# Kernel optimization log

Measured on AMD Instinct MI355X. Metric: run time of the kernel, lower is better.

Reference implementation:

```python
import jax, jax.numpy as jnp
import numpy as np

N, E, NODE_DIM, EDGE_DIM, H, L, G = 50000, 800000, 128, 16, 64, 3, 64


def setup_inputs() -> dict:
    key = jax.random.key(0)
    ks = jax.random.split(key, 20)
    s = 0.05
    inp = {
        "x": jax.random.normal(ks[0], (N, NODE_DIM), jnp.float32),
        "edge_index": jax.random.randint(ks[1], (2, E), 0, N, jnp.int32),
        "edge_attr": jax.random.normal(ks[2], (E, EDGE_DIM), jnp.float32),
        "batch": jnp.sort(jax.random.randint(ks[3], (N,), 0, G, jnp.int32)),
        # node embedding
        "emb_w": jax.random.normal(ks[4], (NODE_DIM, H), jnp.float32) * s,
        "emb_b": jnp.zeros((H,), jnp.float32),
        # per-layer message MLP (stacked over layers)
        "msg_w1": jax.random.normal(ks[5], (L, 2 * H + EDGE_DIM, H), jnp.float32) * s,
        "msg_b1": jnp.zeros((L, H), jnp.float32),
        "msg_w2": jax.random.normal(ks[6], (L, H, H), jnp.float32) * s,
        "msg_b2": jnp.zeros((L, H), jnp.float32),
        # per-layer GRUCell params (torch layout: [3H, H] = [r|z|n])
        "gru_wih": jax.random.normal(ks[7], (L, 3 * H, H), jnp.float32) * s,
        "gru_whh": jax.random.normal(ks[8], (L, 3 * H, H), jnp.float32) * s,
        "gru_bih": jnp.zeros((L, 3 * H), jnp.float32),
        "gru_bhh": jnp.zeros((L, 3 * H), jnp.float32),
        # readout
        "ro_w1": jax.random.normal(ks[9], (H, H), jnp.float32) * s,
        "ro_b1": jnp.zeros((H,), jnp.float32),
        "ro_w2": jax.random.normal(ks[10], (H, 1), jnp.float32) * s,
        "ro_b2": jnp.zeros((1,), jnp.float32),
    }
    return inp


def _layer(x, row, col, edge_attr, w1, b1, w2, b2, wih, whh, bih, bhh):
    # gather-concat-MLP: m is [E, 2H+EDGE_DIM]
    m = jnp.concatenate([x[row], x[col], edge_attr], axis=-1)
    m = jax.nn.relu(m @ w1 + b1) @ w2 + b2  # [E, H]
    agg = jax.ops.segment_sum(m, row, num_segments=N)  # scatter-add -> [N, H]
    # GRUCell(agg, x): gates in torch order r, z, n
    gi = agg @ wih.T + bih  # [N, 3H]
    gh = x @ whh.T + bhh    # [N, 3H]
    r = jax.nn.sigmoid(gi[:, :H] + gh[:, :H])
    z = jax.nn.sigmoid(gi[:, H:2 * H] + gh[:, H:2 * H])
    n = jnp.tanh(gi[:, 2 * H:] + r * gh[:, 2 * H:])
    return (1.0 - z) * n + z * x


def reference(x, edge_index, edge_attr, batch, emb_w, emb_b,
              msg_w1, msg_b1, msg_w2, msg_b2,
              gru_wih, gru_whh, gru_bih, gru_bhh,
              ro_w1, ro_b1, ro_w2, ro_b2):
    row, col = edge_index[0], edge_index[1]
    h = x @ emb_w + emb_b  # node embedding [N, H]
    for l in range(L):
        h = _layer(h, row, col, edge_attr,
                   msg_w1[l], msg_b1[l], msg_w2[l], msg_b2[l],
                   gru_wih[l], gru_whh[l], gru_bih[l], gru_bhh[l])
    # global mean pool over graphs
    sums = jax.ops.segment_sum(h, batch, num_segments=G)
    counts = jax.ops.segment_sum(jnp.ones((N,), h.dtype), batch, num_segments=G)
    g = sums / jnp.maximum(counts, 1.0)[:, None]  # [G, H]
    # readout (dropout is identity in eval mode)
    out = jax.nn.sigmoid(jax.nn.relu(g @ ro_w1 + ro_b1) @ ro_w2 + ro_b2)
    return out  # [G, 1]
```

## Files before the change

### kernel.cpp

```cpp
#include <hip/hip_runtime.h>
#include <cstdint>

#define NN 50000
#define NE 800000
#define HD 64
#define ED 16
#define XD 128
#define NL 3
#define NG 64
#define H3 192
#define POOL_SLICES 16

typedef unsigned int uint32;
typedef unsigned short ushort16;

#if __has_builtin(__builtin_amdgcn_fdot2)
#define USE_DOT2 1
typedef _Float16 v2h __attribute__((ext_vector_type(2)));
#else
#define USE_DOT2 0
#endif

static __device__ __forceinline__ float sigm(float x){ return 1.0f/(1.0f+expf(-x)); }

static __device__ __forceinline__ uint32 f2bf_bits(float f){
  uint32 u = __float_as_uint(f);
  return (u + 0x7fffu + ((u>>16)&1u)) >> 16;
}
static __device__ __forceinline__ uint32 pack2bf(float a, float b){
  return f2bf_bits(a) | (f2bf_bits(b) << 16);
}
static __device__ __forceinline__ float bf_lo(uint32 u){ return __uint_as_float(u << 16); }
static __device__ __forceinline__ float bf_hi(uint32 u){ return __uint_as_float(u & 0xffff0000u); }

#if USE_DOT2
static __device__ __forceinline__ uint32 pack2h(float a, float b){
  v2h p = {(_Float16)a, (_Float16)b};
  return __builtin_bit_cast(uint32, p);
}
static __device__ __forceinline__ float dot2h(uint32 a, uint32 b, float c){
  return __builtin_amdgcn_fdot2(__builtin_bit_cast(v2h, a), __builtin_bit_cast(v2h, b), c, false);
}
#endif

static __device__ __forceinline__ void pre_from_lds(const float* hW, int ldh,
    const float* __restrict__ w1, const float* __restrict__ b1,
    int nb, int lane, float* __restrict__ m1, ushort16* __restrict__ m2b){
  float a1[8] = {0,0,0,0,0,0,0,0};
  float a2[8] = {0,0,0,0,0,0,0,0};
  #pragma unroll 4
  for (int kq=0;kq<HD/4;kq++){
    float wa[4], wb[4];
    #pragma unroll
    for (int q=0;q<4;q++){
      wa[q] = w1[(kq*4+q)*HD + lane];
      wb[q] = w1[(HD+kq*4+q)*HD + lane];
    }
    #pragma unroll
    for (int n=0;n<8;n++){
      float hk[4];
      *(float4*)hk = *(const float4*)&hW[n*ldh + kq*4];
      #pragma unroll
      for (int q=0;q<4;q++){
        a1[n] = fmaf(hk[q], wa[q], a1[n]);
        a2[n] = fmaf(hk[q], wb[q], a2[n]);
      }
    }
  }
  float bb = b1[lane];
  #pragma unroll
  for (int n=0;n<8;n++){
    m1[(size_t)(nb+n)*HD + lane] = a1[n] + bb;
    m2b[(size_t)(nb+n)*HD + lane] = (ushort16)f2bf_bits(a2[n]);
  }
}

__global__ __launch_bounds__(256) void k_embed_pre(const float* __restrict__ x,
    const float* __restrict__ w, const float* __restrict__ b,
    const float* __restrict__ w1_0, const float* __restrict__ b1_0,
    float* __restrict__ h, float* __restrict__ m1, ushort16* __restrict__ m2b){
  __shared__ float xL[4][8][XD];
  int w4 = threadIdx.x >> 6, lane = threadIdx.x & 63;
  int nb = blockIdx.x*32 + w4*8;
  if (nb >= NN) return;
  #pragma unroll
  for (int n=0;n<8;n++){
    xL[w4][n][lane]      = x[(size_t)(nb+n)*XD + lane];
    xL[w4][n][64+lane]   = x[(size_t)(nb+n)*XD + 64 + lane];
  }
  float a[8] = {0,0,0,0,0,0,0,0};
  #pragma unroll 4
  for (int kq=0;kq<XD/4;kq++){
    float wv[4];
    #pragma unroll
    for (int q=0;q<4;q++) wv[q] = w[(kq*4+q)*HD + lane];
    #pragma unroll
    for (int n=0;n<8;n++){
      float xk[4];
      *(float4*)xk = *(const float4*)&xL[w4][n][kq*4];
      #pragma unroll
      for (int q=0;q<4;q++) a[n] = fmaf(xk[q], wv[q], a[n]);
    }
  }
  float bb = b[lane];
  #pragma unroll
  for (int n=0;n<8;n++){
    float hv = a[n] + bb;
    h[(size_t)(nb+n)*HD + lane] = hv;
    xL[w4][n][lane] = hv;
  }
  pre_from_lds(&xL[w4][0][0], XD, w1_0, b1_0, nb, lane, m1, m2b);
}

__global__ __launch_bounds__(256) void k_pre(const float* __restrict__ h,
    const float* __restrict__ w1, const float* __restrict__ b1,
    float* __restrict__ m1, ushort16* __restrict__ m2b){
  __shared__ float hL[4][8][HD];
  int w4 = threadIdx.x >> 6, lane = threadIdx.x & 63;
  int nb = blockIdx.x*32 + w4*8;
  if (nb >= NN) return;
  #pragma unroll
  for (int n=0;n<8;n++) hL[w4][n][lane] = h[(size_t)(nb+n)*HD + lane];
  pre_from_lds(&hL[w4][0][0], HD, w1, b1, nb, lane, m1, m2b);
}

__global__ __launch_bounds__(256) void k_degree(const int* __restrict__ row, int* __restrict__ deg){
  int e = blockIdx.x*blockDim.x + threadIdx.x;
  if (e < NE) atomicAdd(&deg[row[e]], 1);
}

__global__ __launch_bounds__(1024) void k_scan(const int* __restrict__ deg,
    int* __restrict__ row_ptr, int* __restrict__ fill_off){
  __shared__ int wsum[16];
  __shared__ int wexcl[16];
  int t = threadIdx.x, lane = t & 63, wid = t >> 6;
  int running = 0;
  for (int base = 0; base < NN; base += 1024){
    int i = base + t;
    int v = (i < NN) ? deg[i] : 0;
    int s = v;
    #pragma unroll
    for (int off=1; off<64; off<<=1){ int u = __shfl_up(s, off); if (lane>=off) s += u; }
    if (lane==63) wsum[wid] = s;
    __syncthreads();
    if (wid==0){
      int ws = (lane<16) ? wsum[lane] : 0;
      #pragma unroll
      for (int off=1; off<16; off<<=1){ int u = __shfl_up(ws, off); if (lane>=off) ws += u; }
      if (lane<16) wexcl[lane] = ws - wsum[lane];
    }
    __syncthreads();
    int excl = running + wexcl[wid] + (s - v);
    if (i < NN){ row_ptr[i] = excl; fill_off[i] = excl; }
    running += wexcl[15] + wsum[15];
    __syncthreads();
  }
  if (t==0) row_ptr[NN] = running;
}

template<int PERM>
__global__ __launch_bounds__(256) void k_fill(const int* __restrict__ row, const int* __restrict__ colv,
    const float* __restrict__ eattr,
    int* __restrict__ fill_off, int* __restrict__ col_s, int* __restrict__ eid_s,
    ushort16* __restrict__ eattr_b){
  int e = blockIdx.x*blockDim.x + threadIdx.x;
  if (e < NE){
    int r = row[e];
    int p = atomicAdd(&fill_off[r], 1);
    if (PERM){
      col_s[p] = colv[e] << 7;
      const float4* src = (const float4*)(eattr + (size_t)e*ED);
      float4 s0=src[0], s1=src[1], s2=src[2], s3=src[3];
      uint4 d0, d1;
#if USE_DOT2
      d0.x = pack2h(s0.x,s0.y); d0.y = pack2h(s0.z,s0.w);
      d0.z = pack2h(s1.x,s1.y); d0.w = pack2h(s1.z,s1.w);
      d1.x = pack2h(s2.x,s2.y); d1.y = pack2h(s2.z,s2.w);
      d1.z = pack2h(s3.x,s3.y); d1.w = pack2h(s3.z,s3.w);
#else
      d0.x = pack2bf(s0.x,s0.y); d0.y = pack2bf(s0.z,s0.w);
      d0.z = pack2bf(s1.x,s1.y); d0.w = pack2bf(s1.z,s1.w);
      d1.x = pack2bf(s2.x,s2.y); d1.y = pack2bf(s2.z,s2.w);
      d1.z = pack2bf(s3.x,s3.y); d1.w = pack2bf(s3.z,s3.w);
#endif
      uint4* dst = (uint4*)(eattr_b + (size_t)p*ED);
      dst[0] = d0; dst[1] = d1;
    } else {
      col_s[p] = colv[e];
      eid_s[p] = e;
    }
  }
}

__global__ __launch_bounds__(64) void k_fold(const float* __restrict__ w2, const float* __restrict__ b2,
    const float* __restrict__ wih, const float* __restrict__ whh,
    float* __restrict__ Wf, float* __restrict__ WhT, float* __restrict__ bv){
  int bid = blockIdx.x;
  int l = bid / H3, i = bid % H3;
  int k = threadIdx.x;
  const float* w2l  = w2  + (size_t)l*HD*HD;
  const float* wihl = wih + (size_t)l*H3*HD;
  const float* whhl = whh + (size_t)l*H3*HD;
  float acc = 0.f;
  #pragma unroll 8
  for (int m=0;m<HD;m++) acc = fmaf(w2l[k*HD+m], wihl[i*HD+m], acc);
  Wf [(size_t)l*HD*H3 + k*H3 + i] = acc;
  WhT[(size_t)l*HD*H3 + k*H3 + i] = whhl[(size_t)i*HD + k];
  if (k==0){
    float a = 0.f;
    const float* b2l = b2 + l*HD;
    for (int m=0;m<HD;m++) a = fmaf(b2l[m], wihl[i*HD+m], a);
    bv[l*H3 + i] = a;
  }
}

#if USE_DOT2
static __device__ __forceinline__ float edge_term(uint4 ua, uint4 ub, const uint32* wch, float t){
  t = dot2h(ua.x, wch[0], t); t = dot2h(ua.y, wch[1], t);
  t = dot2h(ua.z, wch[2], t); t = dot2h(ua.w, wch[3], t);
  t = dot2h(ub.x, wch[4], t); t = dot2h(ub.y, wch[5], t);
  t = dot2h(ub.z, wch[6], t); t = dot2h(ub.w, wch[7], t);
  return t;
}
#else
static __device__ __forceinline__ float edge_term(uint4 ua, uint4 ub, const float* wch, float t){
  uint32 us[8] = {ua.x,ua.y,ua.z,ua.w,ub.x,ub.y,ub.z,ub.w};
  #pragma unroll
  for (int k=0;k<8;k++){
    t = fmaf(bf_lo(us[k]), wch[2*k],   t);
    t = fmaf(bf_hi(us[k]), wch[2*k+1], t);
  }
  return t;
}
#endif

template<int PERM>
__global__ __launch_bounds__(256) void k_agg(const float* __restrict__ m1, const ushort16* __restrict__ m2b,
    const float* __restrict__ eattr, const ushort16* __restrict__ eattr_b, const float* __restrict__ w1c,
    const int* __restrict__ row_ptr, const int* __restrict__ col_s, const int* __restrict__ eid_s,
    float* __restrict__ tsum){
  int lane = threadIdx.x & 63;
  int wid_v = blockIdx.x*4 + (threadIdx.x>>6);
  int wid = __builtin_amdgcn_readfirstlane(wid_v);
  if (wid >= NN) return;
  float base = m1[(size_t)wid*HD + lane];
  int s     = __builtin_amdgcn_readfirstlane(row_ptr[wid]);
  int e_end = __builtin_amdgcn_readfirstlane(row_ptr[wid+1]);
  float ts0=0.f, ts1=0.f, ts2=0.f, ts3=0.f;
  int idx = s;
  if (PERM){
    const char* mb = (const char*)m2b;
    uint32 l2 = (uint32)lane * 2u;
#if USE_DOT2
    uint32 wch[8];
    #pragma unroll
    for (int k=0;k<8;k++) wch[k] = pack2h(w1c[(2*k)*HD + lane], w1c[(2*k+1)*HD + lane]);
#else
    float wch[ED];
    #pragma unroll
    for (int k=0;k<ED;k++) wch[k] = w1c[k*HD + lane];
#endif
    for (; idx + 8 <= e_end; idx += 8){
      int c0 = col_s[idx+0], c1 = col_s[idx+1], c2 = col_s[idx+2], c3 = col_s[idx+3];
      int c4 = col_s[idx+4], c5 = col_s[idx+5], c6 = col_s[idx+6], c7 = col_s[idx+7];
      unsigned short g0 = *(const unsigned short*)(mb + (uint32)c0 + l2);
      unsigned short g1 = *(const unsigned short*)(mb + (uint32)c1 + l2);
      unsigned short g2 = *(const unsigned short*)(mb + (uint32)c2 + l2);
      unsigned short g3 = *(const unsigned short*)(mb + (uint32)c3 + l2);
      unsigned short g4 = *(const unsigned short*)(mb + (uint32)c4 + l2);
      unsigned short g5 = *(const unsigned short*)(mb + (uint32)c5 + l2);
      unsigned short g6 = *(const unsigned short*)(mb + (uint32)c6 + l2);
      unsigned short g7 = *(const unsigned short*)(mb + (uint32)c7 + l2);
      const uint4* ea = (const uint4*)(eattr_b + (size_t)idx*ED);
      uint4 e0=ea[0],  e1=ea[1],  e2=ea[2],  e3=ea[3];
      uint4 e4=ea[4],  e5=ea[5],  e6=ea[6],  e7=ea[7];
      uint4 e8=ea[8],  e9=ea[9],  e10=ea[10],e11=ea[11];
      uint4 e12=ea[12],e13=ea[13],e14=ea[14],e15=ea[15];
      ts0 += fmaxf(edge_term(e0,  e1,  wch, base + bf_lo(g0)), 0.f);
      ts1 += fmaxf(edge_term(e2,  e3,  wch, base + bf_lo(g1)), 0.f);
      ts2 += fmaxf(edge_term(e4,  e5,  wch, base + bf_lo(g2)), 0.f);
      ts3 += fmaxf(edge_term(e6,  e7,  wch, base + bf_lo(g3)), 0.f);
      ts0 += fmaxf(edge_term(e8,  e9,  wch, base + bf_lo(g4)), 0.f);
      ts1 += fmaxf(edge_term(e10, e11, wch, base + bf_lo(g5)), 0.f);
      ts2 += fmaxf(edge_term(e12, e13, wch, base + bf_lo(g6)), 0.f);
      ts3 += fmaxf(edge_term(e14, e15, wch, base + bf_lo(g7)), 0.f);
    }
    if (idx + 4 <= e_end){
      int c0 = col_s[idx+0], c1 = col_s[idx+1], c2 = col_s[idx+2], c3 = col_s[idx+3];
      unsigned short g0 = *(const unsigned short*)(mb + (uint32)c0 + l2);
      unsigned short g1 = *(const unsigned short*)(mb + (uint32)c1 + l2);
      unsigned short g2 = *(const unsigned short*)(mb + (uint32)c2 + l2);
      unsigned short g3 = *(const unsigned short*)(mb + (uint32)c3 + l2);
      const uint4* ea = (const uint4*)(eattr_b + (size_t)idx*ED);
      uint4 e0=ea[0], e1=ea[1], e2=ea[2], e3=ea[3];
      uint4 e4=ea[4], e5=ea[5], e6=ea[6], e7=ea[7];
      ts0 += fmaxf(edge_term(e0, e1, wch, base + bf_lo(g0)), 0.f);
      ts1 += fmaxf(edge_term(e2, e3, wch, base + bf_lo(g1)), 0.f);
      ts2 += fmaxf(edge_term(e4, e5, wch, base + bf_lo(g2)), 0.f);
      ts3 += fmaxf(edge_term(e6, e7, wch, base + bf_lo(g3)), 0.f);
      idx += 4;
    }
    for (; idx < e_end; idx++){
      int c = col_s[idx];
      unsigned short g = *(const unsigned short*)(mb + (uint32)c + l2);
      const uint4* ea = (const uint4*)(eattr_b + (size_t)idx*ED);
      uint4 e0 = ea[0], e1 = ea[1];
      ts0 += fmaxf(edge_term(e0, e1, wch, base + bf_lo(g)), 0.f);
    }
  } else {
    float wc[ED];
    #pragma unroll
    for (int k=0;k<ED;k++) wc[k] = w1c[k*HD + lane];
    for (; idx < e_end; idx++){
      int c = col_s[idx];
      int e = eid_s[idx];
      const float4* ea4 = (const float4*)(eattr + (size_t)e*ED);
      float4 a0 = ea4[0], a1 = ea4[1], a2 = ea4[2], a3 = ea4[3];
      float t = base + bf_lo((uint32)m2b[(size_t)c*HD + lane]);
      t = fmaf(a0.x, wc[0],  t); t = fmaf(a0.y, wc[1],  t);
      t = fmaf(a0.z, wc[2],  t); t = fmaf(a0.w, wc[3],  t);
      t = fmaf(a1.x, wc[4],  t); t = fmaf(a1.y, wc[5],  t);
      t = fmaf(a1.z, wc[6],  t); t = fmaf(a1.w, wc[7],  t);
      t = fmaf(a2.x, wc[8],  t); t = fmaf(a2.y, wc[9],  t);
      t = fmaf(a2.z, wc[10], t); t = fmaf(a2.w, wc[11], t);
      t = fmaf(a3.x, wc[12], t); t = fmaf(a3.y, wc[13], t);
      t = fmaf(a3.z, wc[14], t); t = fmaf(a3.w, wc[15], t);
      ts0 += fmaxf(t, 0.f);
    }
  }
  tsum[(size_t)wid*HD + lane] = (ts0 + ts1) + (ts2 + ts3);
}

__global__ __launch_bounds__(256) void k_gru(float* __restrict__ h, const float* __restrict__ tsum,
    const int* __restrict__ row_ptr,
    const float* __restrict__ Wf, const float* __restrict__ WhT,
    const float* __restrict__ bv, const float* __restrict__ bih, const float* __restrict__ bhh){
  __shared__ float tsL[4][8][HD];
  __shared__ float hL[4][8][HD];
  int w4 = threadIdx.x >> 6, lane = threadIdx.x & 63;
  int nb = blockIdx.x*32 + w4*8;
  if (nb >= NN) return;
  #pragma unroll
  for (int n=0;n<8;n++){
    tsL[w4][n][lane] = tsum[(size_t)(nb+n)*HD + lane];
    hL[w4][n][lane]  = h[(size_t)(nb+n)*HD + lane];
  }
  float gr[8]={0,0,0,0,0,0,0,0}, gz[8]={0,0,0,0,0,0,0,0}, gn[8]={0,0,0,0,0,0,0,0};
  float pr[8]={0,0,0,0,0,0,0,0}, pz[8]={0,0,0,0,0,0,0,0}, pn[8]={0,0,0,0,0,0,0,0};
  #pragma unroll 2
  for (int kq=0;kq<HD/4;kq++){
    const float* wf = Wf  + (size_t)(kq*4)*H3;
    const float* wh = WhT + (size_t)(kq*4)*H3;
    float wfr[4],wfz[4],wfn[4],whr[4],whz[4],whn[4];
    #pragma unroll
    for (int q=0;q<4;q++){
      wfr[q]=wf[q*H3+lane]; wfz[q]=wf[q*H3+HD+lane]; wfn[q]=wf[q*H3+2*HD+lane];
      whr[q]=wh[q*H3+lane]; whz[q]=wh[q*H3+HD+lane]; whn[q]=wh[q*H3+2*HD+lane];
    }
    #pragma unroll
    for (int n=0;n<8;n++){
      float tk[4], hk[4];
      *(float4*)tk = *(const float4*)&tsL[w4][n][kq*4];
      *(float4*)hk = *(const float4*)&hL[w4][n][kq*4];
      #pragma unroll
      for (int q=0;q<4;q++){
        gr[n]=fmaf(tk[q],wfr[q],gr[n]); gz[n]=fmaf(tk[q],wfz[q],gz[n]); gn[n]=fmaf(tk[q],wfn[q],gn[n]);
        pr[n]=fmaf(hk[q],whr[q],pr[n]); pz[n]=fmaf(hk[q],whz[q],pz[n]); pn[n]=fmaf(hk[q],whn[q],pn[n]);
      }
    }
  }
  float bvr=bv[lane], bvz=bv[HD+lane], bvn=bv[2*HD+lane];
  float bir=bih[lane], biz=bih[HD+lane], bin=bih[2*HD+lane];
  float bhr=bhh[lane], bhz=bhh[HD+lane], bhn=bhh[2*HD+lane];
  int rp0 = row_ptr[nb];
  #pragma unroll
  for (int n=0;n<8;n++){
    int rp1 = row_ptr[nb+n+1];
    float deg = (float)(rp1 - rp0);
    rp0 = rp1;
    float r  = sigm(gr[n]+pr[n] + deg*bvr + bir + bhr);
    float z  = sigm(gz[n]+pz[n] + deg*bvz + biz + bhz);
    float nv = tanhf(gn[n] + deg*bvn + bin + r*(pn[n] + bhn));
    float hv = hL[w4][n][lane];
    h[(size_t)(nb+n)*HD + lane] = (1.f - z)*nv + z*hv;
  }
}

__global__ __launch_bounds__(256) void k_pool(const float* __restrict__ h, const int* __restrict__ batch,
    float* __restrict__ gsum, float* __restrict__ gcnt){
  __shared__ int rng[2];
  __shared__ float red[4][HD];
  int g = blockIdx.x / POOL_SLICES;
  int slice = blockIdx.x % POOL_SLICES;
  int t = threadIdx.x, lane = t & 63, w = t >> 6;
  if (t < 2){
    int target = g + t;
    int lo = 0, hi = NN;
    while (lo < hi){ int mid = (lo + hi) >> 1; if (batch[mid] < target) lo = mid + 1; else hi = mid; }
    rng[t] = lo;
  }
  __syncthreads();
  int start = rng[0], end = rng[1];
  if (slice == 0 && t == 0) gcnt[g] = (float)(end - start);
  int len = end - start;
  int per = (len + POOL_SLICES - 1) / POOL_SLICES;
  int s0 = start + slice * per;
  int s1 = min(s0 + per, end);
  float acc = 0.f;
  for (int n = s0 + w; n < s1; n += 4) acc += h[(size_t)n*HD + lane];
  red[w][lane] = acc;
  __syncthreads();
  if (w == 0){
    float v = red[0][lane] + red[1][lane] + red[2][lane] + red[3][lane];
    atomicAdd(&gsum[g*HD + lane], v);
  }
}

__global__ __launch_bounds__(64) void k_readout(const float* __restrict__ gsum, const float* __restrict__ gcnt,
    const float* __restrict__ w1, const float* __restrict__ b1,
    const float* __restrict__ w2, const float* __restrict__ b2, float* __restrict__ out){
  int g = blockIdx.x;
  int lane = threadIdx.x;
  float c = fmaxf(gcnt[g], 1.0f);
  float gm = gsum[g*HD + lane] / c;
  float a = b1[lane];
  for (int k=0;k<HD;k++) a = fmaf(__shfl(gm, k), w1[k*HD + lane], a);
  a = fmaxf(a, 0.f);
  float p = a * w2[lane];
  #pragma unroll
  for (int off=32; off>0; off>>=1) p += __shfl_down(p, off);
  if (lane==0) out[g] = 1.f/(1.f + expf(-(p + b2[0])));
}

extern "C" void kernel_launch(void* const* d_in, const int* in_sizes, int n_in,
                              void* d_out, int out_size, void* d_ws, size_t ws_size,
                              hipStream_t stream){
  const float* x        = (const float*)d_in[0];
  const int*   eidx     = (const int*)d_in[1];
  const float* eattr    = (const float*)d_in[2];
  const int*   batch    = (const int*)d_in[3];
  const float* emb_w    = (const float*)d_in[4];
  const float* emb_b    = (const float*)d_in[5];
  const float* msg_w1   = (const float*)d_in[6];
  const float* msg_b1   = (const float*)d_in[7];
  const float* msg_w2   = (const float*)d_in[8];
  const float* msg_b2   = (const float*)d_in[9];
  const float* gru_wih  = (const float*)d_in[10];
  const float* gru_whh  = (const float*)d_in[11];
  const float* gru_bih  = (const float*)d_in[12];
  const float* gru_bhh  = (const float*)d_in[13];
  const float* ro_w1    = (const float*)d_in[14];
  const float* ro_b1    = (const float*)d_in[15];
  const float* ro_w2    = (const float*)d_in[16];
  const float* ro_b2    = (const float*)d_in[17];
  float* out = (float*)d_out;

  char* p = (char*)d_ws;
  size_t used = 0;
  auto alloc = [&](size_t bytes)->void*{
    void* r = (void*)p; size_t rb = (bytes + 255) & ~(size_t)255; p += rb; used += rb; return r;
  };
  float*     h    = (float*)alloc((size_t)NN*HD*4);
  float*     m1   = (float*)alloc((size_t)NN*HD*4);
  ushort16*  m2b  = (ushort16*)alloc((size_t)NN*HD*2);
  float*     tsum = (float*)alloc((size_t)NN*HD*4);
  int*       deg  = (int*)  alloc((size_t)NN*4);
  int*       rowp = (int*)  alloc((size_t)(NN+1)*4);
  int*       foff = (int*)  alloc((size_t)NN*4);
  int*       col_s= (int*)  alloc((size_t)NE*4);
  int*       eid_s= (int*)  alloc((size_t)NE*4);
  float*     Wf   = (float*)alloc((size_t)NL*HD*H3*4);
  float*     WhT  = (float*)alloc((size_t)NL*HD*H3*4);
  float*     bv   = (float*)alloc((size_t)NL*H3*4);
  float*     gsum = (float*)alloc((size_t)NG*HD*4);
  float*     gcnt = (float*)alloc((size_t)NG*4);
  size_t ea_bytes = (size_t)NE*ED*2;
  bool perm = (used + ea_bytes + 256) <= ws_size;
  ushort16* eattr_b = perm ? (ushort16*)alloc(ea_bytes) : nullptr;

  const int* row = eidx;
  const int* col = eidx + NE;

  hipMemsetAsync(deg,  0, (size_t)NN*4, stream);
  hipMemsetAsync(gsum, 0, (size_t)NG*HD*4, stream);

  const int nb32 = (NN + 31)/32;
  const int nbw  = (NN + 3)/4;
  const int nbe  = (NE + 255)/256;

  k_degree<<<nbe, 256, 0, stream>>>(row, deg);
  k_scan  <<<1, 1024, 0, stream>>>(deg, rowp, foff);
  if (perm) k_fill<1><<<nbe, 256, 0, stream>>>(row, col, eattr, foff, col_s, eid_s, eattr_b);
  else      k_fill<0><<<nbe, 256, 0, stream>>>(row, col, eattr, foff, col_s, eid_s, eattr_b);
  k_fold  <<<NL*H3, 64, 0, stream>>>(msg_w2, msg_b2, gru_wih, gru_whh, Wf, WhT, bv);
  k_embed_pre<<<nb32, 256, 0, stream>>>(x, emb_w, emb_b, msg_w1, msg_b1, h, m1, m2b);

  for (int l=0; l<NL; l++){
    const float* w1l = msg_w1 + (size_t)l*(2*HD+ED)*HD;
    if (l > 0){
      k_pre<<<nb32, 256, 0, stream>>>(h, w1l, msg_b1 + l*HD, m1, m2b);
    }
    if (perm) k_agg<1><<<nbw, 256, 0, stream>>>(m1, m2b, eattr, eattr_b, w1l + (size_t)2*HD*HD,
                                                rowp, col_s, eid_s, tsum);
    else      k_agg<0><<<nbw, 256, 0, stream>>>(m1, m2b, eattr, eattr_b, w1l + (size_t)2*HD*HD,
                                                rowp, col_s, eid_s, tsum);
    k_gru<<<nb32, 256, 0, stream>>>(h, tsum, rowp,
                                    Wf + (size_t)l*HD*H3, WhT + (size_t)l*HD*H3,
                                    bv + l*H3, gru_bih + l*H3, gru_bhh + l*H3);
  }

  k_pool   <<<NG*POOL_SLICES, 256, 0, stream>>>(h, batch, gsum, gcnt);
  k_readout<<<NG, 64, 0, stream>>>(gsum, gcnt, ro_w1, ro_b1, ro_w2, ro_b2, out);
}
```

Baseline: 530.4 us.

## Pack dense weights to bf16 pairs and stage them in LDS per block

Adds a packing kernel that converts the embedding and message-MLP node weights to bf16 pairs, and changes the fold kernel to emit the GRU weights in the same packed form. The embed, pre and GRU kernels now copy these packed weights cooperatively into shared memory once per block and read them from LDS, instead of each wave reloading fp32 weights from global or L2. This halves weight bytes and cuts redundant global traffic, at the cost of bf16 weight precision, more LDS per block (about 48KB in k_gru), lower occupancy, and an added __syncthreads.

```diff
diff --git a/kernel.cpp b/kernel.cpp
--- a/kernel.cpp
+++ b/kernel.cpp
@@ -43,19 +43,34 @@
 }
 #endif
 
-static __device__ __forceinline__ void pre_from_lds(const float* hW, int ldh,
-    const float* __restrict__ w1, const float* __restrict__ b1,
+__global__ __launch_bounds__(256) void k_packw(const float* __restrict__ emb_w,
+    const float* __restrict__ msg_w1,
+    uint32* __restrict__ embP, uint32* __restrict__ W1aP, uint32* __restrict__ W1bP){
+  int idx = blockIdx.x*256 + threadIdx.x;
+  if (idx < 4096){
+    int kp = idx>>6, c = idx&63;
+    embP[idx] = pack2bf(emb_w[(2*kp)*HD+c], emb_w[(2*kp+1)*HD+c]);
+  }
+  int j = idx - 4096;
+  if (j >= 0 && j < NL*2048){
+    int l = j >> 11; int r = j & 2047; int kp = r>>6, c = r&63;
+    const float* base = msg_w1 + (size_t)l*(2*HD+ED)*HD;
+    W1aP[j] = pack2bf(base[(2*kp)*HD+c],      base[(2*kp+1)*HD+c]);
+    W1bP[j] = pack2bf(base[(HD+2*kp)*HD+c],   base[(HD+2*kp+1)*HD+c]);
+  }
+}
+
+static __device__ __forceinline__ void pre_from_lds_p(const float* hW, int ldh,
+    const uint32* aL, const uint32* bL, const float* __restrict__ b1,
     int nb, int lane, float* __restrict__ m1, ushort16* __restrict__ m2b){
   float a1[8] = {0,0,0,0,0,0,0,0};
   float a2[8] = {0,0,0,0,0,0,0,0};
   #pragma unroll 4
   for (int kq=0;kq<HD/4;kq++){
-    float wa[4], wb[4];
-    #pragma unroll
-    for (int q=0;q<4;q++){
-      wa[q] = w1[(kq*4+q)*HD + lane];
-      wb[q] = w1[(HD+kq*4+q)*HD + lane];
-    }
+    uint32 pa0 = aL[(2*kq)*HD + lane], pa1 = aL[(2*kq+1)*HD + lane];
+    uint32 pb0 = bL[(2*kq)*HD + lane], pb1 = bL[(2*kq+1)*HD + lane];
+    float wa[4] = {bf_lo(pa0), bf_hi(pa0), bf_lo(pa1), bf_hi(pa1)};
+    float wb[4] = {bf_lo(pb0), bf_hi(pb0), bf_lo(pb1), bf_hi(pb1)};
     #pragma unroll
     for (int n=0;n<8;n++){
       float hk[4];
@@ -76,24 +91,40 @@
 }
 
 __global__ __launch_bounds__(256) void k_embed_pre(const float* __restrict__ x,
-    const float* __restrict__ w, const float* __restrict__ b,
-    const float* __restrict__ w1_0, const float* __restrict__ b1_0,
+    const uint32* __restrict__ embP, const float* __restrict__ b,
+    const uint32* __restrict__ aP, const uint32* __restrict__ bP, const float* __restrict__ b1_0,
     float* __restrict__ h, float* __restrict__ m1, ushort16* __restrict__ m2b){
-  __shared__ float xL[4][8][XD];
-  int w4 = threadIdx.x >> 6, lane = threadIdx.x & 63;
+  __shared__ float  xL[4][8][XD];
+  __shared__ uint32 embL[64*64];
+  __shared__ uint32 aL[32*64];
+  __shared__ uint32 bL[32*64];
+  int t = threadIdx.x;
+  {
+    const uint4* ge = (const uint4*)embP;
+    const uint4* ga = (const uint4*)aP;
+    const uint4* gb = (const uint4*)bP;
+    uint4* se = (uint4*)embL; uint4* sa = (uint4*)aL; uint4* sb = (uint4*)bL;
+    #pragma unroll
+    for (int i=0;i<4;i++) se[t + i*256] = ge[t + i*256];
+    #pragma unroll
+    for (int i=0;i<2;i++){ sa[t + i*256] = ga[t + i*256]; sb[t + i*256] = gb[t + i*256]; }
+  }
+  int w4 = t >> 6, lane = t & 63;
   int nb = blockIdx.x*32 + w4*8;
+  if (nb < NN){
+    #pragma unroll
+    for (int n=0;n<8;n++){
+      xL[w4][n][lane]      = x[(size_t)(nb+n)*XD + lane];
+      xL[w4][n][64+lane]   = x[(size_t)(nb+n)*XD + 64 + lane];
+    }
+  }
+  __syncthreads();
   if (nb >= NN) return;
-  #pragma unroll
-  for (int n=0;n<8;n++){
-    xL[w4][n][lane]      = x[(size_t)(nb+n)*XD + lane];
-    xL[w4][n][64+lane]   = x[(size_t)(nb+n)*XD + 64 + lane];
-  }
   float a[8] = {0,0,0,0,0,0,0,0};
   #pragma unroll 4
   for (int kq=0;kq<XD/4;kq++){
-    float wv[4];
-    #pragma unroll
-    for (int q=0;q<4;q++) wv[q] = w[(kq*4+q)*HD + lane];
+    uint32 p0 = embL[(2*kq)*HD + lane], p1 = embL[(2*kq+1)*HD + lane];
+    float wv[4] = {bf_lo(p0), bf_hi(p0), bf_lo(p1), bf_hi(p1)};
     #pragma unroll
     for (int n=0;n<8;n++){
       float xk[4];
@@ -109,19 +140,32 @@
     h[(size_t)(nb+n)*HD + lane] = hv;
     xL[w4][n][lane] = hv;
   }
-  pre_from_lds(&xL[w4][0][0], XD, w1_0, b1_0, nb, lane, m1, m2b);
+  pre_from_lds_p(&xL[w4][0][0], XD, aL, bL, b1_0, nb, lane, m1, m2b);
 }
 
 __global__ __launch_bounds__(256) void k_pre(const float* __restrict__ h,
-    const float* __restrict__ w1, const float* __restrict__ b1,
+    const uint32* __restrict__ aP, const uint32* __restrict__ bP, const float* __restrict__ b1,
     float* __restrict__ m1, ushort16* __restrict__ m2b){
-  __shared__ float hL[4][8][HD];
-  int w4 = threadIdx.x >> 6, lane = threadIdx.x & 63;
+  __shared__ float  hL[4][8][HD];
+  __shared__ uint32 aL[32*64];
+  __shared__ uint32 bL[32*64];
+  int t = threadIdx.x;
+  {
+    const uint4* ga = (const uint4*)aP;
+    const uint4* gb = (const uint4*)bP;
+    uint4* sa = (uint4*)aL; uint4* sb = (uint4*)bL;
+    #pragma unroll
+    for (int i=0;i<2;i++){ sa[t + i*256] = ga[t + i*256]; sb[t + i*256] = gb[t + i*256]; }
+  }
+  int w4 = t >> 6, lane = t & 63;
   int nb = blockIdx.x*32 + w4*8;
+  if (nb < NN){
+    #pragma unroll
+    for (int n=0;n<8;n++) hL[w4][n][lane] = h[(size_t)(nb+n)*HD + lane];
+  }
+  __syncthreads();
   if (nb >= NN) return;
-  #pragma unroll
-  for (int n=0;n<8;n++) hL[w4][n][lane] = h[(size_t)(nb+n)*HD + lane];
-  pre_from_lds(&hL[w4][0][0], HD, w1, b1, nb, lane, m1, m2b);
+  pre_from_lds_p(&hL[w4][0][0], HD, aL, bL, b1, nb, lane, m1, m2b);
 }
 
 __global__ __launch_bounds__(256) void k_degree(const int* __restrict__ row, int* __restrict__ deg){
@@ -194,7 +238,7 @@
 
 __global__ __launch_bounds__(64) void k_fold(const float* __restrict__ w2, const float* __restrict__ b2,
     const float* __restrict__ wih, const float* __restrict__ whh,
-    float* __restrict__ Wf, float* __restrict__ WhT, float* __restrict__ bv){
+    uint32* __restrict__ WfP, uint32* __restrict__ WhP, float* __restrict__ bv){
   int bid = blockIdx.x;
   int l = bid / H3, i = bid % H3;
   int k = threadIdx.x;
@@ -204,8 +248,13 @@
   float acc = 0.f;
   #pragma unroll 8
   for (int m=0;m<HD;m++) acc = fmaf(w2l[k*HD+m], wihl[i*HD+m], acc);
-  Wf [(size_t)l*HD*H3 + k*H3 + i] = acc;
-  WhT[(size_t)l*HD*H3 + k*H3 + i] = whhl[(size_t)i*HD + k];
+  float wh = whhl[(size_t)i*HD + k];
+  float accN = __shfl_down(acc, 1);
+  float whN  = __shfl_down(wh, 1);
+  if ((k & 1) == 0){
+    WfP[((size_t)l*32 + (k>>1))*H3 + i] = pack2bf(acc, accN);
+    WhP[((size_t)l*32 + (k>>1))*H3 + i] = pack2bf(wh, whN);
+  }
   if (k==0){
     float a = 0.f;
     const float* b2l = b2 + l*HD;
@@ -333,30 +382,49 @@
 
 __global__ __launch_bounds__(256) void k_gru(float* __restrict__ h, const float* __restrict__ tsum,
     const int* __restrict__ row_ptr,
-    const float* __restrict__ Wf, const float* __restrict__ WhT,
+    const uint32* __restrict__ WfP, const uint32* __restrict__ WhP,
     const float* __restrict__ bv, const float* __restrict__ bih, const float* __restrict__ bhh){
+  __shared__ uint32 wfL[32*H3];
+  __shared__ uint32 whL[32*H3];
   __shared__ float tsL[4][8][HD];
   __shared__ float hL[4][8][HD];
-  int w4 = threadIdx.x >> 6, lane = threadIdx.x & 63;
+  int t = threadIdx.x;
+  {
+    const uint4* gf = (const uint4*)WfP;
+    const uint4* gh = (const uint4*)WhP;
+    uint4* sf = (uint4*)wfL; uint4* sh = (uint4*)whL;
+    #pragma unroll
+    for (int i=0;i<6;i++){ int j = t + i*256; sf[j] = gf[j]; sh[j] = gh[j]; }
+  }
+  int w4 = t >> 6, lane = t & 63;
   int nb = blockIdx.x*32 + w4*8;
+  if (nb < NN){
+    #pragma unroll
+    for (int n=0;n<8;n++){
+      tsL[w4][n][lane] = tsum[(size_t)(nb+n)*HD + lane];
+      hL[w4][n][lane]  = h[(size_t)(nb+n)*HD + lane];
+    }
+  }
+  __syncthreads();
   if (nb >= NN) return;
-  #pragma unroll
-  for (int n=0;n<8;n++){
-    tsL[w4][n][lane] = tsum[(size_t)(nb+n)*HD + lane];
-    hL[w4][n][lane]  = h[(size_t)(nb+n)*HD + lane];
-  }
   float gr[8]={0,0,0,0,0,0,0,0}, gz[8]={0,0,0,0,0,0,0,0}, gn[8]={0,0,0,0,0,0,0,0};
   float pr[8]={0,0,0,0,0,0,0,0}, pz[8]={0,0,0,0,0,0,0,0}, pn[8]={0,0,0,0,0,0,0,0};
   #pragma unroll 2
   for (int kq=0;kq<HD/4;kq++){
-    const float* wf = Wf  + (size_t)(kq*4)*H3;
-    const float* wh = WhT + (size_t)(kq*4)*H3;
-    float wfr[4],wfz[4],wfn[4],whr[4],whz[4],whn[4];
-    #pragma unroll
-    for (int q=0;q<4;q++){
-      wfr[q]=wf[q*H3+lane]; wfz[q]=wf[q*H3+HD+lane]; wfn[q]=wf[q*H3+2*HD+lane];
-      whr[q]=wh[q*H3+lane]; whz[q]=wh[q*H3+HD+lane]; whn[q]=wh[q*H3+2*HD+lane];
-    }
+    const uint32* f0 = wfL + (2*kq)*H3;
+    const uint32* f1 = wfL + (2*kq+1)*H3;
+    const uint32* h0 = whL + (2*kq)*H3;
+    const uint32* h1 = whL + (2*kq+1)*H3;
+    uint32 ufr0=f0[lane], ufz0=f0[64+lane], ufn0=f0[128+lane];
+    uint32 ufr1=f1[lane], ufz1=f1[64+lane], ufn1=f1[128+lane];
+    uint32 uhr0=h0[lane], uhz0=h0[64+lane], uhn0=h0[128+lane];
+    uint32 uhr1=h1[lane], uhz1=h1[64+lane], uhn1=h1[128+lane];
+    float wfr[4]={bf_lo(ufr0),bf_hi(ufr0),bf_lo(ufr1),bf_hi(ufr1)};
+    float wfz[4]={bf_lo(ufz0),bf_hi(ufz0),bf_lo(ufz1),bf_hi(ufz1)};
+    float wfn[4]={bf_lo(ufn0),bf_hi(ufn0),bf_lo(ufn1),bf_hi(ufn1)};
+    float whr[4]={bf_lo(uhr0),bf_hi(uhr0),bf_lo(uhr1),bf_hi(uhr1)};
+    float whz[4]={bf_lo(uhz0),bf_hi(uhz0),bf_lo(uhz1),bf_hi(uhz1)};
+    float whn[4]={bf_lo(uhn0),bf_hi(uhn0),bf_lo(uhn1),bf_hi(uhn1)};
     #pragma unroll
     for (int n=0;n<8;n++){
       float tk[4], hk[4];
@@ -469,9 +537,12 @@
   int*       foff = (int*)  alloc((size_t)NN*4);
   int*       col_s= (int*)  alloc((size_t)NE*4);
   int*       eid_s= (int*)  alloc((size_t)NE*4);
-  float*     Wf   = (float*)alloc((size_t)NL*HD*H3*4);
-  float*     WhT  = (float*)alloc((size_t)NL*HD*H3*4);
+  uint32*    WfP  = (uint32*)alloc((size_t)NL*32*H3*4);
+  uint32*    WhP  = (uint32*)alloc((size_t)NL*32*H3*4);
   float*     bv   = (float*)alloc((size_t)NL*H3*4);
+  uint32*    embP = (uint32*)alloc((size_t)4096*4);
+  uint32*    W1aP = (uint32*)alloc((size_t)NL*2048*4);
+  uint32*    W1bP = (uint32*)alloc((size_t)NL*2048*4);
   float*     gsum = (float*)alloc((size_t)NG*HD*4);
   float*     gcnt = (float*)alloc((size_t)NG*4);
   size_t ea_bytes = (size_t)NE*ED*2;
@@ -492,20 +563,22 @@
   k_scan  <<<1, 1024, 0, stream>>>(deg, rowp, foff);
   if (perm) k_fill<1><<<nbe, 256, 0, stream>>>(row, col, eattr, foff, col_s, eid_s, eattr_b);
   else      k_fill<0><<<nbe, 256, 0, stream>>>(row, col, eattr, foff, col_s, eid_s, eattr_b);
-  k_fold  <<<NL*H3, 64, 0, stream>>>(msg_w2, msg_b2, gru_wih, gru_whh, Wf, WhT, bv);
-  k_embed_pre<<<nb32, 256, 0, stream>>>(x, emb_w, emb_b, msg_w1, msg_b1, h, m1, m2b);
+  k_fold  <<<NL*H3, 64, 0, stream>>>(msg_w2, msg_b2, gru_wih, gru_whh, WfP, WhP, bv);
+  k_packw <<<64, 256, 0, stream>>>(emb_w, msg_w1, embP, W1aP, W1bP);
+  k_embed_pre<<<nb32, 256, 0, stream>>>(x, embP, emb_b, W1aP, W1bP, msg_b1, h, m1, m2b);
 
   for (int l=0; l<NL; l++){
     const float* w1l = msg_w1 + (size_t)l*(2*HD+ED)*HD;
     if (l > 0){
-      k_pre<<<nb32, 256, 0, stream>>>(h, w1l, msg_b1 + l*HD, m1, m2b);
+      k_pre<<<nb32, 256, 0, stream>>>(h, W1aP + (size_t)l*2048, W1bP + (size_t)l*2048,
+                                      msg_b1 + l*HD, m1, m2b);
     }
     if (perm) k_agg<1><<<nbw, 256, 0, stream>>>(m1, m2b, eattr, eattr_b, w1l + (size_t)2*HD*HD,
                                                 rowp, col_s, eid_s, tsum);
     else      k_agg<0><<<nbw, 256, 0, stream>>>(m1, m2b, eattr, eattr_b, w1l + (size_t)2*HD*HD,
                                                 rowp, col_s, eid_s, tsum);
     k_gru<<<nb32, 256, 0, stream>>>(h, tsum, rowp,
-                                    Wf + (size_t)l*HD*H3, WhT + (size_t)l*HD*H3,
+                                    WfP + (size_t)l*32*H3, WhP + (size_t)l*32*H3,
                                     bv + l*H3, gru_bih + l*H3, gru_bhh + l*H3);
   }
 
```

After: 550.4 us. +3.8%, slower.
